# Kernel tuning notes

Hardware: AMD Instinct MI355X
Metric: run time of the kernel (lower is better)

The kernel has to match this reference:

```python
import jax, jax.numpy as jnp
import numpy as np

ACT_BIT = 8
BETA = 0.9
N_LEVELS = (1 << ACT_BIT) - 1  # 255
N_ITERS = 80
LP_P = 2.4


def _quant_dequant(t, mn, mx):
    """Asymmetric uniform quantize-dequantize to ACT_BIT bits over [mn, mx]."""
    delta = jnp.maximum(mx - mn, 1e-8) / N_LEVELS
    zp = jnp.round(-mn / delta)
    q = jnp.clip(jnp.round(t / delta) + zp, 0.0, float(N_LEVELS))
    return (q - zp) * delta


def setup_inputs() -> dict:
    key = jax.random.key(0)
    kx, = jax.random.split(key, 1)
    x = jax.random.normal(kx, (32, 512, 32, 32), dtype=jnp.float32)
    x_min_buf = jnp.zeros((1,), dtype=jnp.float32)
    x_max_buf = jnp.zeros((1,), dtype=jnp.float32)
    return {"x": x, "x_min_buf": x_min_buf, "x_max_buf": x_max_buf}


def reference(x, x_min_buf, x_max_buf):
    xd = jax.lax.stop_gradient(x)
    x_min = jnp.min(xd)
    x_max = jnp.max(xd)

    # 80-candidate MSE (p=2.4) range search over shrinking factors 1.0 .. 0.21
    def score_fn(i):
        f = 1.0 - i * 0.01
        mn = x_min * f
        mx = x_max * f
        qa = _quant_dequant(xd, mn, mx)
        return jnp.mean(jnp.abs(qa - xd) ** LP_P)

    idx = jnp.arange(N_ITERS, dtype=x.dtype)
    scores = jax.lax.map(score_fn, idx)
    best = jnp.argmin(scores)  # ties -> first, matching 'score < best_score'
    factor = 1.0 - best.astype(x.dtype) * 0.01
    save_min = x_min * factor
    save_max = x_max * factor

    # EMA buffer update (buffers start at 0)
    new_min = x_min_buf[0] * BETA + save_min * (1.0 - BETA)
    new_max = x_max_buf[0] * BETA + save_max * (1.0 - BETA)

    # final quantization with updated range (STE-style in torch; fwd is plain quant-dequant)
    return _quant_dequant(x, new_min, new_max)
```

## Files before the change

kernel.cpp:

```cpp
#include <hip/hip_runtime.h>
#include <math.h>

#define NCAND 80
#define NEXACT 7
#define NPT 8
#define NPTQ 4
#define TAU 3.5f
#define TAILSLOTS 16
#define MMSLOTS 2048
#define SUBBLOCKS 256
#define CGRP 4
#define NCPB (NCAND / CGRP)

#if defined(__HIP_DEVICE_COMPILE__) && __has_builtin(__builtin_amdgcn_exp2f)
#define EXP2F(x) __builtin_amdgcn_exp2f(x)
#else
#define EXP2F(x) exp2f(x)
#endif
#if defined(__HIP_DEVICE_COMPILE__) && __has_builtin(__builtin_amdgcn_logf)
#define LOG2F(x) __builtin_amdgcn_logf(x)
#else
#define LOG2F(x) log2f(x)
#endif

#define LOAD_FENCE() asm volatile("" ::: "memory")

struct WS {
  unsigned int ctr_sel, ctr_exact;
  int sel_base;
  float xmin_f, xmax_f;
  unsigned int pad0[3];
  double sub_scores[NCAND];
  double tail_scores[NCAND];
  double exact_scores[NEXACT + 1];
  float4 sel[NEXACT];
  float4 final_params;
  unsigned int bneg_ord[MMSLOTS];
  unsigned int bmax_ord[MMSLOTS];
  float tail[MMSLOTS * TAILSLOTS];
};

__device__ __forceinline__ unsigned int f2o(float f) {
  unsigned int u = __float_as_uint(f);
  return (u & 0x80000000u) ? ~u : (u | 0x80000000u);
}
__device__ __forceinline__ float o2f(unsigned int o) {
  unsigned int u = (o & 0x80000000u) ? (o ^ 0x80000000u) : ~o;
  return __uint_as_float(u);
}

__device__ __forceinline__ float4 cand_params(float xmin, float xmax, int c) {
  float f  = 1.0f - (float)c * 0.01f;
  float mn = xmin * f, mx = xmax * f;
  float delta = fmaxf(mx - mn, 1e-8f) / 255.0f;
  float zp = rintf(-mn / delta);
  return make_float4(delta, 1.0f / delta, -zp, 255.0f - zp);
}

__device__ __forceinline__ float powp(float x, float4 k) {
  float r = fminf(fmaxf(rintf(x * k.y), k.z), k.w);
  float e = fabsf(fmaf(r, k.x, -x));
  return EXP2F(2.4f * LOG2F(e));
}

__global__ __launch_bounds__(256) void k_minmax(const float4* __restrict__ x4, int n4, WS* ws) {
  __shared__ float stail[TAILSLOTS];
  __shared__ unsigned int scnt;
  if (threadIdx.x == 0) scnt = 0u;
  __syncthreads();

  float4 v[NPT];
  int base = blockIdx.x * (256 * NPT) + threadIdx.x;
  if ((blockIdx.x + 1) * (256 * NPT) <= n4) {
    #pragma unroll
    for (int j = 0; j < NPT; j++) v[j] = x4[base + j * 256];
  } else {
    #pragma unroll
    for (int j = 0; j < NPT; j++) {
      int i = base + j * 256;
      v[j] = (i < n4) ? x4[i] : make_float4(0.f, 0.f, 0.f, 0.f);
    }
  }
  LOAD_FENCE();

  float mn = INFINITY, mx = -INFINITY;
  #pragma unroll
  for (int j = 0; j < NPT; j++) {
    mn = fminf(mn, fminf(fminf(v[j].x, v[j].y), fminf(v[j].z, v[j].w)));
    mx = fmaxf(mx, fmaxf(fmaxf(v[j].x, v[j].y), fmaxf(v[j].z, v[j].w)));
  }

  if (__any(mx > TAU || mn < -TAU)) {
    #pragma unroll
    for (int j = 0; j < NPT; j++) {
      float a[4] = {v[j].x, v[j].y, v[j].z, v[j].w};
      #pragma unroll
      for (int q = 0; q < 4; q++) {
        if (fabsf(a[q]) > TAU) {
          unsigned int p = atomicAdd(&scnt, 1u);
          if (p < TAILSLOTS) stail[p] = a[q];
        }
      }
    }
  }

  #pragma unroll
  for (int off = 32; off; off >>= 1) {
    mn = fminf(mn, __shfl_xor(mn, off));
    mx = fmaxf(mx, __shfl_xor(mx, off));
  }
  __shared__ float smn[4], smx[4];
  int wid = threadIdx.x >> 6;
  if ((threadIdx.x & 63) == 0) { smn[wid] = mn; smx[wid] = mx; }
  __syncthreads();
  if (threadIdx.x == 0) {
    mn = fminf(fminf(smn[0], smn[1]), fminf(smn[2], smn[3]));
    mx = fmaxf(fmaxf(smx[0], smx[1]), fmaxf(smx[2], smx[3]));
    ws->bneg_ord[blockIdx.x] = f2o(-mn);
    ws->bmax_ord[blockIdx.x] = f2o(mx);
    if (scnt > TAILSLOTS) scnt = TAILSLOTS;
  }
  __syncthreads();
  if (threadIdx.x < TAILSLOTS) {
    ws->tail[blockIdx.x * TAILSLOTS + threadIdx.x] =
        (threadIdx.x < scnt) ? stail[threadIdx.x] : 0.0f;
  }
}

__global__ __launch_bounds__(256) void k_subtail(const float4* __restrict__ x4, int n4, int nmm, WS* ws) {
  unsigned int rn = 0u, rx = 0u;
  for (int i = threadIdx.x; i < nmm; i += 256) {
    unsigned int a = ws->bneg_ord[i], b = ws->bmax_ord[i];
    rn = (a > rn) ? a : rn;
    rx = (b > rx) ? b : rx;
  }
  #pragma unroll
  for (int off = 32; off; off >>= 1) {
    unsigned int a = __shfl_xor(rn, off), b = __shfl_xor(rx, off);
    rn = (a > rn) ? a : rn;
    rx = (b > rx) ? b : rx;
  }
  __shared__ unsigned int sred[2][4];
  int wid = threadIdx.x >> 6, lane = threadIdx.x & 63;
  if (lane == 0) { sred[0][wid] = rn; sred[1][wid] = rx; }
  __syncthreads();
  rn = sred[0][0]; rx = sred[1][0];
  #pragma unroll
  for (int w = 1; w < 4; w++) {
    rn = (sred[0][w] > rn) ? sred[0][w] : rn;
    rx = (sred[1][w] > rx) ? sred[1][w] : rx;
  }
  float xmin = -o2f(rn), xmax = o2f(rx);

  bool is_sub = blockIdx.x < SUBBLOCKS * CGRP;
  int rel   = is_sub ? blockIdx.x : blockIdx.x - SUBBLOCKS * CGRP;
  int slice = rel >> 2;
  int grp   = rel & 3;
  int cbase = grp * NCPB;

  __shared__ float4 cc[NCPB];
  if (threadIdx.x < NCPB) cc[threadIdx.x] = cand_params(xmin, xmax, cbase + threadIdx.x);
  __syncthreads();

  __shared__ float part[4][NCPB];

  if (is_sub) {
    float xv[8];
    #pragma unroll
    for (int j = 0; j < 2; j++) {
      int s = j * (SUBBLOCKS * 256) + slice * 256 + threadIdx.x;
      int d = (s >> 8) * 8192 + (s & 255);
      float4 v = (d < n4) ? x4[d] : make_float4(0.f, 0.f, 0.f, 0.f);
      float a[4] = {v.x, v.y, v.z, v.w};
      #pragma unroll
      for (int q = 0; q < 4; q++)
        xv[4 * j + q] = (fabsf(a[q]) <= TAU) ? a[q] : 0.0f;
    }
    LOAD_FENCE();
    #pragma unroll 1
    for (int c = 0; c < NCPB; c++) {
      float4 k = cc[c];
      float s0 = 0.f, s1 = 0.f;
      #pragma unroll
      for (int e = 0; e < 8; e += 2) {
        s0 += powp(xv[e], k);
        s1 += powp(xv[e + 1], k);
      }
      float s = s0 + s1;
      #pragma unroll
      for (int off = 32; off; off >>= 1) s += __shfl_xor(s, off);
      if (lane == 0) part[wid][c] = s;
    }
    __syncthreads();
    if (threadIdx.x < NCPB) {
      double tot = (double)part[0][threadIdx.x] + (double)part[1][threadIdx.x]
                 + (double)part[2][threadIdx.x] + (double)part[3][threadIdx.x];
      atomicAdd(&ws->sub_scores[cbase + threadIdx.x], tot);
    }
  } else {
    int i = slice * 256 + threadIdx.x;
    float xval = (i < nmm * TAILSLOTS) ? ws->tail[i] : 0.0f;
    #pragma unroll 1
    for (int c = 0; c < NCPB; c++) {
      float s = powp(xval, cc[c]);
      #pragma unroll
      for (int off = 32; off; off >>= 1) s += __shfl_xor(s, off);
      if (lane == 0) part[wid][c] = s;
    }
    __syncthreads();
    if (threadIdx.x < NCPB) {
      double tot = (double)part[0][threadIdx.x] + (double)part[1][threadIdx.x]
                 + (double)part[2][threadIdx.x] + (double)part[3][threadIdx.x];
      atomicAdd(&ws->tail_scores[cbase + threadIdx.x], tot);
    }
  }
  __syncthreads();
  if (threadIdx.x == 0) {
    __threadfence();
    unsigned int t = atomicAdd(&ws->ctr_sel, 1u);
    if (t == gridDim.x - 1) {
      __threadfence();
      double best = 1e300; int bi = 0;
      for (int c = 0; c < NCAND; c++) {
        double s = 32.0 * __hip_atomic_load(&ws->sub_scores[c], __ATOMIC_RELAXED, __HIP_MEMORY_SCOPE_AGENT)
                 + __hip_atomic_load(&ws->tail_scores[c], __ATOMIC_RELAXED, __HIP_MEMORY_SCOPE_AGENT);
        if (s < best) { best = s; bi = c; }
      }
      int lo = bi - (NEXACT / 2);
      if (lo < 0) lo = 0;
      if (lo > NCAND - NEXACT) lo = NCAND - NEXACT;
      ws->sel_base = lo;
      ws->xmin_f = xmin; ws->xmax_f = xmax;
      for (int j = 0; j < NEXACT; j++) ws->sel[j] = cand_params(xmin, xmax, lo + j);
    }
  }
}

__global__ __launch_bounds__(256) void k_exact(const float4* __restrict__ x4, int n4, WS* ws,
                                               const float* __restrict__ minbuf,
                                               const float* __restrict__ maxbuf) {
  __shared__ float4 cc[NEXACT];
  if (threadIdx.x < NEXACT) cc[threadIdx.x] = ws->sel[threadIdx.x];
  __syncthreads();

  float xv[4 * NPT];
  int base = blockIdx.x * (256 * NPT) + threadIdx.x;
  if ((blockIdx.x + 1) * (256 * NPT) <= n4) {
    #pragma unroll
    for (int j = 0; j < NPT; j++) {
      float4 v = x4[base + j * 256];
      xv[4 * j + 0] = v.x; xv[4 * j + 1] = v.y;
      xv[4 * j + 2] = v.z; xv[4 * j + 3] = v.w;
    }
  } else {
    #pragma unroll
    for (int j = 0; j < NPT; j++) {
      int i = base + j * 256;
      float4 v = (i < n4) ? x4[i] : make_float4(0.f, 0.f, 0.f, 0.f);
      xv[4 * j + 0] = v.x; xv[4 * j + 1] = v.y;
      xv[4 * j + 2] = v.z; xv[4 * j + 3] = v.w;
    }
  }
  LOAD_FENCE();

  __shared__ float part[4][NEXACT];
  int wid = threadIdx.x >> 6, lane = threadIdx.x & 63;

  #pragma unroll 1
  for (int c = 0; c < NEXACT; c++) {
    float4 k = cc[c];
    float s0 = 0.f, s1 = 0.f, s2 = 0.f, s3 = 0.f;
    #pragma unroll
    for (int e = 0; e < 4 * NPT; e += 4) {
      s0 += powp(xv[e], k);
      s1 += powp(xv[e + 1], k);
      s2 += powp(xv[e + 2], k);
      s3 += powp(xv[e + 3], k);
    }
    float s = (s0 + s1) + (s2 + s3);
    #pragma unroll
    for (int off = 32; off; off >>= 1) s += __shfl_xor(s, off);
    if (lane == 0) part[wid][c] = s;
  }
  __syncthreads();
  if (threadIdx.x < NEXACT) {
    double tot = (double)part[0][threadIdx.x] + (double)part[1][threadIdx.x]
               + (double)part[2][threadIdx.x] + (double)part[3][threadIdx.x];
    atomicAdd(&ws->exact_scores[threadIdx.x], tot);
  }
  __syncthreads();
  if (threadIdx.x == 0) {
    __threadfence();
    unsigned int t = atomicAdd(&ws->ctr_exact, 1u);
    if (t == gridDim.x - 1) {
      __threadfence();
      double best = 1e300; int bj = 0;
      for (int j = 0; j < NEXACT; j++) {
        double s = __hip_atomic_load(&ws->exact_scores[j], __ATOMIC_RELAXED, __HIP_MEMORY_SCOPE_AGENT);
        if (s < best) { best = s; bj = j; }
      }
      int c = ws->sel_base + bj;
      float factor = 1.0f - (float)c * 0.01f;
      float xmin = ws->xmin_f, xmax = ws->xmax_f;
      float save_min = xmin * factor, save_max = xmax * factor;
      float new_min = minbuf[0] * 0.9f + save_min * 0.1f;
      float new_max = maxbuf[0] * 0.9f + save_max * 0.1f;
      float delta = fmaxf(new_max - new_min, 1e-8f) / 255.0f;
      float zp = rintf(-new_min / delta);
      ws->final_params = make_float4(delta, 1.0f / delta, -zp, 255.0f - zp);
    }
  }
}

__global__ __launch_bounds__(256) void k_quant(const float4* __restrict__ x4, float4* __restrict__ o4,
                                               int n4, const WS* __restrict__ ws) {
  float4 k = ws->final_params;
  float4 v[NPTQ];
  int base = blockIdx.x * (256 * NPTQ) + threadIdx.x;
  if ((blockIdx.x + 1) * (256 * NPTQ) <= n4) {
    #pragma unroll
    for (int j = 0; j < NPTQ; j++) v[j] = x4[base + j * 256];
    LOAD_FENCE();
    #pragma unroll
    for (int j = 0; j < NPTQ; j++) {
      float4 o;
      o.x = fminf(fmaxf(rintf(v[j].x * k.y), k.z), k.w) * k.x;
      o.y = fminf(fmaxf(rintf(v[j].y * k.y), k.z), k.w) * k.x;
      o.z = fminf(fmaxf(rintf(v[j].z * k.y), k.z), k.w) * k.x;
      o.w = fminf(fmaxf(rintf(v[j].w * k.y), k.z), k.w) * k.x;
      o4[base + j * 256] = o;
    }
  } else {
    #pragma unroll
    for (int j = 0; j < NPTQ; j++) {
      int i = base + j * 256;
      if (i < n4) {
        float4 vv = x4[i];
        float4 o;
        o.x = fminf(fmaxf(rintf(vv.x * k.y), k.z), k.w) * k.x;
        o.y = fminf(fmaxf(rintf(vv.y * k.y), k.z), k.w) * k.x;
        o.z = fminf(fmaxf(rintf(vv.z * k.y), k.z), k.w) * k.x;
        o.w = fminf(fmaxf(rintf(vv.w * k.y), k.z), k.w) * k.x;
        o4[i] = o;
      }
    }
  }
}

extern "C" void kernel_launch(void* const* d_in, const int* in_sizes, int n_in,
                              void* d_out, int out_size, void* d_ws, size_t ws_size,
                              hipStream_t stream) {
  const float* x      = (const float*)d_in[0];
  const float* minbuf = (const float*)d_in[1];
  const float* maxbuf = (const float*)d_in[2];
  float* out = (float*)d_out;
  WS* ws = (WS*)d_ws;
  int n  = in_sizes[0];
  int n4 = n / 4;

  hipMemsetAsync(ws, 0, offsetof(WS, bneg_ord), stream);

  int mmBlocks = (n4 + 256 * NPT - 1) / (256 * NPT);
  if (mmBlocks > MMSLOTS) mmBlocks = MMSLOTS;
  k_minmax<<<mmBlocks, 256, 0, stream>>>((const float4*)x, n4, ws);

  int tailSlices = (mmBlocks * TAILSLOTS + 255) / 256;
  int stBlocks = (SUBBLOCKS + tailSlices) * CGRP;
  k_subtail<<<stBlocks, 256, 0, stream>>>((const float4*)x, n4, mmBlocks, ws);

  k_exact<<<mmBlocks, 256, 0, stream>>>((const float4*)x, n4, ws, minbuf, maxbuf);

  int qBlocks = (n4 + 256 * NPTQ - 1) / (256 * NPTQ);
  k_quant<<<qBlocks, 256, 0, stream>>>((const float4*)x, (float4*)out, n4, ws);
}
```

Before: 132.6 us.

## Shrink exact refinement window, fuse candidate loop, zero workspace in-kernel

Cuts the number of candidates scored exactly from 7 to 5 around the approximate best. Restructures the exact-scoring loop so each element is loaded once and scored against all candidates held in registers, instead of one pass per candidate. Removes the separate memset launch by having block 0 of the min/max kernel zero the header counters and score accumulators. A narrower window risks missing the true argmin if the approximate scores are off by more than two candidates, and in-kernel zeroing relies on those fields not being read by other min/max blocks before block 0 clears them.

```diff
diff --git a/kernel.cpp b/kernel.cpp
--- a/kernel.cpp
+++ b/kernel.cpp
@@ -2,7 +2,7 @@
 #include <math.h>
 
 #define NCAND 80
-#define NEXACT 7
+#define NEXACT 5
 #define NPT 8
 #define NPTQ 4
 #define TAU 3.5f
@@ -32,13 +32,14 @@
   unsigned int pad0[3];
   double sub_scores[NCAND];
   double tail_scores[NCAND];
-  double exact_scores[NEXACT + 1];
+  double exact_scores[NEXACT + 3];
   float4 sel[NEXACT];
   float4 final_params;
   unsigned int bneg_ord[MMSLOTS];
   unsigned int bmax_ord[MMSLOTS];
   float tail[MMSLOTS * TAILSLOTS];
 };
+#define HDR_DOUBLES (2 * NCAND + NEXACT + 3)
 
 __device__ __forceinline__ unsigned int f2o(float f) {
   unsigned int u = __float_as_uint(f);
@@ -67,6 +68,11 @@
   __shared__ float stail[TAILSLOTS];
   __shared__ unsigned int scnt;
   if (threadIdx.x == 0) scnt = 0u;
+  if (blockIdx.x == 0) {
+    if (threadIdx.x < 8) ((unsigned int*)ws)[threadIdx.x] = 0u;
+    double* hd = ws->sub_scores;
+    for (int i = threadIdx.x; i < HDR_DOUBLES; i += 256) hd[i] = 0.0;
+  }
   __syncthreads();
 
   float4 v[NPT];
@@ -239,9 +245,9 @@
 __global__ __launch_bounds__(256) void k_exact(const float4* __restrict__ x4, int n4, WS* ws,
                                                const float* __restrict__ minbuf,
                                                const float* __restrict__ maxbuf) {
-  __shared__ float4 cc[NEXACT];
-  if (threadIdx.x < NEXACT) cc[threadIdx.x] = ws->sel[threadIdx.x];
-  __syncthreads();
+  float4 kk[NEXACT];
+  #pragma unroll
+  for (int c = 0; c < NEXACT; c++) kk[c] = ws->sel[c];
 
   float xv[4 * NPT];
   int base = blockIdx.x * (256 * NPT) + threadIdx.x;
@@ -263,21 +269,21 @@
   }
   LOAD_FENCE();
 
+  float acc[NEXACT];
+  #pragma unroll
+  for (int c = 0; c < NEXACT; c++) acc[c] = 0.f;
+  #pragma unroll
+  for (int e = 0; e < 4 * NPT; e++) {
+    float x = xv[e];
+    #pragma unroll
+    for (int c = 0; c < NEXACT; c++) acc[c] += powp(x, kk[c]);
+  }
+
   __shared__ float part[4][NEXACT];
   int wid = threadIdx.x >> 6, lane = threadIdx.x & 63;
-
-  #pragma unroll 1
+  #pragma unroll
   for (int c = 0; c < NEXACT; c++) {
-    float4 k = cc[c];
-    float s0 = 0.f, s1 = 0.f, s2 = 0.f, s3 = 0.f;
-    #pragma unroll
-    for (int e = 0; e < 4 * NPT; e += 4) {
-      s0 += powp(xv[e], k);
-      s1 += powp(xv[e + 1], k);
-      s2 += powp(xv[e + 2], k);
-      s3 += powp(xv[e + 3], k);
-    }
-    float s = (s0 + s1) + (s2 + s3);
+    float s = acc[c];
     #pragma unroll
     for (int off = 32; off; off >>= 1) s += __shfl_xor(s, off);
     if (lane == 0) part[wid][c] = s;
@@ -358,8 +364,6 @@
   int n  = in_sizes[0];
   int n4 = n / 4;
 
-  hipMemsetAsync(ws, 0, offsetof(WS, bneg_ord), stream);
-
   int mmBlocks = (n4 + 256 * NPT - 1) / (256 * NPT);
   if (mmBlocks > MMSLOTS) mmBlocks = MMSLOTS;
   k_minmax<<<mmBlocks, 256, 0, stream>>>((const float4*)x, n4, ws);
```

New measurement: 143.7 us. 8.4% more time.
